# Optimization experiments

Hardware: AMD Instinct MI355X
Metric: run time of the kernel (lower is better)

## Reference

```python
import jax, jax.numpy as jnp
import numpy as np

VOCAB, D = 6000, 256  # vocab_size, units
B, L = 64, 2048


def setup_inputs() -> dict:
    key = jax.random.key(0)
    k1, k2, k3, k4, k5 = jax.random.split(key, 5)
    context = jax.random.randint(k1, (B, L), 0, VOCAB)  # 0 = pad/mask id
    emb = jax.random.normal(k2, (VOCAB, D), dtype=jnp.float32) * 0.05
    # Keras LSTM packs gates as [i, f, c, o] along the last axis (4*D)
    W = jax.random.normal(k3, (D, 4 * D), dtype=jnp.float32) * (1.0 / np.sqrt(D))
    U = jax.random.normal(k4, (D, 4 * D), dtype=jnp.float32) * (1.0 / np.sqrt(D))
    b = jnp.concatenate([
        jnp.zeros((D,), jnp.float32),
        jnp.ones((D,), jnp.float32),   # unit_forget_bias=True default in Keras
        jnp.zeros((2 * D,), jnp.float32),
    ])
    return {"context": context, "emb": emb, "W": W, "U": U, "b": b}


def reference(context, emb, W, U, b):
    mask = context != 0                       # (B, L) mask_zero semantics
    x = emb[context]                          # (B, L, D) embedding lookup
    xg = jnp.einsum("bld,dg->blg", x, W) + b  # (B, L, 4D) input-to-gate, precomputed

    h0 = jnp.zeros((context.shape[0], D), xg.dtype)
    c0 = h0

    def step(carry, inp):
        h, c = carry
        xg_t, m = inp                          # (B, 4D), (B,)
        g = xg_t + h @ U                       # (B, 4D)
        i, f, cand, o = jnp.split(g, 4, axis=-1)
        i = jax.nn.sigmoid(i)
        f = jax.nn.sigmoid(f)
        o = jax.nn.sigmoid(o)
        c_new = f * c + i * jnp.tanh(cand)
        h_new = o * jnp.tanh(c_new)
        m = m[:, None]
        # Keras masking: masked steps carry previous state/output forward
        h = jnp.where(m, h_new, h)
        c = jnp.where(m, c_new, c)
        return (h, c), h

    xs = (jnp.swapaxes(xg, 0, 1), jnp.swapaxes(mask, 0, 1))  # time-major for scan
    (_, _), hs = jax.lax.scan(step, (h0, c0), xs)
    return jnp.swapaxes(hs, 0, 1)             # (B, L, D)
```

## Files before the change

### kernel.cpp

```cpp
#include <hip/hip_runtime.h>
#include <hip/hip_bf16.h>


#define B_     64
#define L_     2048
#define D_     256
#define G4_    1024
#define VOCAB_ 6000

typedef short    s16x8 __attribute__((ext_vector_type(8)));
typedef float    f32x4 __attribute__((ext_vector_type(4)));
typedef unsigned u32x2 __attribute__((ext_vector_type(2)));
typedef unsigned u32x4 __attribute__((ext_vector_type(4)));

#define OFF_EMBB   0u
#define OFF_WT     3072000u
#define OFF_UF     3596288u
#define OFF_HTAG   4120576u
#define OFF_DONE   4251648u
#define OFF_XG     4251712u
#define WS_NEED    272687168u

#define ULDS_OFF   0
#define SG_OFF     65536
#define HL_OFF     82432
#define ROLE_OFF   90624
#define SMEM_TOTAL 90752

__global__ void prep_kernel(const float* __restrict__ emb,
                            const float* __restrict__ W,
                            const float* __restrict__ U,
                            __hip_bfloat16* __restrict__ embb,
                            __hip_bfloat16* __restrict__ Wt,
                            __hip_bfloat16* __restrict__ Ufrag) {
  const int stride = gridDim.x * blockDim.x;
  const int i0 = blockIdx.x * blockDim.x + threadIdx.x;
  for (int i = i0; i < VOCAB_ * D_; i += stride)
    embb[i] = __float2bfloat16(emb[i]);
  for (int i = i0; i < D_ * G4_; i += stride) {
    int k = i >> 10;
    int n = i & (G4_ - 1);
    Wt[n * D_ + k] = __float2bfloat16(W[i]);
  }
  for (int i = i0; i < 262144; i += stride) {
    int j  = i & 7;
    int l  = (i >> 3) & 63;
    int fr = i >> 9;
    int nt = fr & 1;
    int kk = (fr >> 1) & 7;
    int w  = (fr >> 4) & 7;
    int qq = fr >> 7;
    int n = (w >> 1) * 256 + qq * 64 + (w & 1) * 32 + nt * 16 + (l & 15);
    int k = kk * 32 + (l >> 4) * 8 + j;
    Ufrag[i] = __float2bfloat16(U[k * G4_ + n]);
  }
}

__global__ void mask_kernel(const int* __restrict__ ctx,
                            unsigned char* __restrict__ m8) {
  const int stride = gridDim.x * blockDim.x;
  for (int i = blockIdx.x * blockDim.x + threadIdx.x; i < B_ * L_; i += stride) {
    int b = i & 63, t = i >> 6;
    m8[t * 64 + b] = (ctx[b * L_ + t] != 0) ? 1 : 0;
  }
}

__device__ inline unsigned pk2(float a, float b) {
  return (unsigned)__bfloat16_as_ushort(__float2bfloat16(a)) |
         ((unsigned)__bfloat16_as_ushort(__float2bfloat16(b)) << 16);
}
__device__ inline float bl(unsigned u) {
  union { unsigned u; float f; } c; c.u = u << 16; return c.f;
}
__device__ inline float bh(unsigned u) {
  union { unsigned u; float f; } c; c.u = u & 0xffff0000u; return c.f;
}
__device__ inline float fsigmoid(float x) { return 1.f / (1.f + __expf(-x)); }
__device__ inline float ftanh(float x)    { return 1.f - 2.f / (__expf(2.f * x) + 1.f); }

__global__ __launch_bounds__(256, 2)
void xg_kernel(const int* __restrict__ ctx,
               const __hip_bfloat16* __restrict__ embb,
               const __hip_bfloat16* __restrict__ Wt,
               unsigned* __restrict__ xgw) {
  const int bid = blockIdx.x;
  const int Q   = bid & 3;
  const int g   = (bid >> 2) & 3;
  const int tc  = bid >> 4;
  const int tid = threadIdx.x;
  const int wv  = tid >> 6;
  const int l   = tid & 63;
  const int l15 = l & 15, lhi = l >> 4;
  const int row0 = g * 16;

  s16x8 bfr[8][4];
#pragma unroll
  for (int nt = 0; nt < 4; ++nt) {
    const int n = Q * 256 + wv * 64 + nt * 16 + l15;
    const __hip_bfloat16* wp = Wt + n * D_ + lhi * 8;
#pragma unroll
    for (int kk = 0; kk < 8; ++kk)
      bfr[kk][nt] = *(const s16x8*)(wp + kk * 32);
  }

  for (int tt = 0; tt < 64; ++tt) {
    const int t = tc * 64 + tt;
    const int tok = ctx[(row0 + l15) * L_ + t];
    const __hip_bfloat16* xp = embb + tok * D_ + lhi * 8;
    s16x8 af[8];
#pragma unroll
    for (int kk = 0; kk < 8; ++kk)
      af[kk] = *(const s16x8*)(xp + kk * 32);

    f32x4 acc[4];
#pragma unroll
    for (int nt = 0; nt < 4; ++nt) acc[nt] = (f32x4){0.f, 0.f, 0.f, 0.f};
#pragma unroll
    for (int kk = 0; kk < 8; ++kk)
#pragma unroll
      for (int nt = 0; nt < 4; ++nt)
        acc[nt] = __builtin_amdgcn_mfma_f32_16x16x32_bf16(af[kk], bfr[kk][nt], acc[nt], 0, 0, 0);

#pragma unroll
    for (int nt = 0; nt < 4; ++nt)
#pragma unroll
      for (int r = 0; r < 4; ++r) {
        float nb = __shfl_xor(acc[nt][r], 1);
        if (!(l15 & 1)) {
          unsigned v = pk2(acc[nt][r], nb);
          int em = lhi * 4 + r;
          int p  = nt * 8 + (l15 >> 1);
          size_t idx = ((((size_t)(t * 4 + g) * 4 + wv) * 16 + em) * 32 + p) * 4 + Q;
          xgw[idx] = v;
        }
      }
  }
}

__global__ __launch_bounds__(512, 1)
void scan_kernel(const float* __restrict__ bias,
                 const __hip_bfloat16* __restrict__ Ufrag,
                 const unsigned* __restrict__ xgw,
                 const unsigned char* __restrict__ mask8,
                 unsigned* __restrict__ donef,
                 char* __restrict__ htag,
                 float* __restrict__ out) {
  extern __shared__ __align__(16) char smem[];
  const int bid = blockIdx.x;
  const int tid = threadIdx.x;

  if (bid >= 16) {
    volatile int* hd = (volatile int*)(smem + ROLE_OFF);
    if (tid == 0) *hd = 0;
    __syncthreads();
    float v0 = (float)(tid + 1), v1 = v0 * 1.1f, v2 = v0 * 1.2f, v3 = v0 * 1.3f;
    for (int it = 0; it < (1 << 15); ++it) {
#pragma unroll
      for (int kk = 0; kk < 128; ++kk) {
        v0 = __builtin_fmaf(v0, 1.0000001f, 1.0e-7f);
        v1 = __builtin_fmaf(v1, 1.0000001f, 1.0e-7f);
        v2 = __builtin_fmaf(v2, 1.0000001f, 1.0e-7f);
        v3 = __builtin_fmaf(v3, 1.0000001f, 1.0e-7f);
      }
      if (tid == 0 && (it & 3) == 0) {
        u32x4 fa, fb, fc, fd;
        asm volatile(
            "global_load_dwordx4 %0, %4, off sc0 sc1\n\t"
            "global_load_dwordx4 %1, %4, off offset:16 sc0 sc1\n\t"
            "global_load_dwordx4 %2, %4, off offset:32 sc0 sc1\n\t"
            "global_load_dwordx4 %3, %4, off offset:48 sc0 sc1\n\t"
            "s_waitcnt vmcnt(0)"
            : "=&v"(fa), "=&v"(fb), "=&v"(fc), "=&v"(fd)
            : "v"(donef) : "memory");
        unsigned mn = fa.x;
        mn = fa.y < mn ? fa.y : mn; mn = fa.z < mn ? fa.z : mn; mn = fa.w < mn ? fa.w : mn;
        mn = fb.x < mn ? fb.x : mn; mn = fb.y < mn ? fb.y : mn;
        mn = fb.z < mn ? fb.z : mn; mn = fb.w < mn ? fb.w : mn;
        mn = fc.x < mn ? fc.x : mn; mn = fc.y < mn ? fc.y : mn;
        mn = fc.z < mn ? fc.z : mn; mn = fc.w < mn ? fc.w : mn;
        mn = fd.x < mn ? fd.x : mn; mn = fd.y < mn ? fd.y : mn;
        mn = fd.z < mn ? fd.z : mn; mn = fd.w < mn ? fd.w : mn;
        if (mn != 0u) *hd = 1;
      }
      if (*hd) break;
    }
    asm volatile("" :: "v"(v0), "v"(v1), "v"(v2), "v"(v3));
    return;
  }

  const int g = bid >> 2;
  const int q = bid & 3;
  const int row0 = g * 16;

  const int w   = tid >> 6;
  const int l   = tid & 63;
  const int l15 = l & 15, lhi = l >> 4;
  const int Q   = w >> 1, sgs = w & 1;
  const int em  = tid >> 5;
  const int e5  = tid & 31;

  s16x8* ulds = (s16x8*)(smem + ULDS_OFF);
  float* sg   = (float*)(smem + SG_OFF);
  char*  hl   = smem + HL_OFF;

  const s16x8* ufb = (const s16x8*)Ufrag + (size_t)((q * 8 + w) * 16) * 64;
  s16x8 ur[8];
#pragma unroll
  for (int jf = 0; jf < 8; ++jf)
    ur[jf] = ufb[jf * 64 + l];
#pragma unroll
  for (int jf = 0; jf < 8; ++jf)
    ulds[(w * 8 + jf) * 64 + l] = ufb[(8 + jf) * 64 + l];

  float bq[4][2];
#pragma unroll
  for (int Qq = 0; Qq < 4; ++Qq) {
    bq[Qq][0] = bias[Qq * 256 + q * 64 + 2 * e5];
    bq[Qq][1] = bias[Qq * 256 + q * 64 + 2 * e5 + 1];
  }

  float cc[2] = {0.f, 0.f}, hh[2] = {0.f, 0.f};
  __syncthreads();

  const int prow = w * 2 + (l >> 5);
  const int pswz = (prow & 7) << 4;

  for (int t = 0; t < L_; ++t) {
    const u32x4 xq = *(const u32x4*)(xgw +
        (((((size_t)t * 4 + g) * 4 + q) * 16 + em) * 32 + e5) * 4);
    const unsigned char mk = mask8[t * 64 + row0 + em];

    {
      const char* hp = htag + ((t + 1) & 1) * 65536 + (row0 + prow) * 1024 + (l & 31) * 32;
      const unsigned want = (unsigned)t;
      u32x4 qa, qb;
      int spins = 0;
      while (true) {
        asm volatile("global_load_dwordx4 %0, %2, off sc0 sc1\n\t"
                     "global_load_dwordx4 %1, %2, off offset:16 sc0 sc1\n\t"
                     "s_waitcnt vmcnt(0)"
                     : "=&v"(qa), "=&v"(qb) : "v"(hp) : "memory");
        unsigned mn = qa.y < qa.w ? qa.y : qa.w;
        mn = qb.y < mn ? qb.y : mn;
        mn = qb.w < mn ? qb.w : mn;
        if (__all((int)(mn >= want))) break;
        if (++spins > 16384) break;
      }
      union { unsigned u[4]; s16x8 v; } hcv;
      hcv.u[0] = qa.x; hcv.u[1] = qa.z; hcv.u[2] = qb.x; hcv.u[3] = qb.z;
      *(s16x8*)(hl + prow * 512 + (((l & 31) * 16) ^ pswz)) = hcv.v;
    }
    asm volatile("s_waitcnt lgkmcnt(0)" ::: "memory");
    __builtin_amdgcn_s_barrier();

    f32x4 acc0 = {0.f, 0.f, 0.f, 0.f}, acc1 = {0.f, 0.f, 0.f, 0.f};
    s16x8 hf[8];
#pragma unroll
    for (int kk = 0; kk < 8; ++kk)
      hf[kk] = *(const s16x8*)(hl + l15 * 512 + ((kk * 64 + lhi * 16) ^ ((l15 & 7) << 4)));
#pragma unroll
    for (int kk = 0; kk < 4; ++kk) {
      acc0 = __builtin_amdgcn_mfma_f32_16x16x32_bf16(hf[kk], ur[kk * 2 + 0], acc0, 0, 0, 0);
      acc1 = __builtin_amdgcn_mfma_f32_16x16x32_bf16(hf[kk], ur[kk * 2 + 1], acc1, 0, 0, 0);
    }
#pragma unroll
    for (int kk = 4; kk < 8; ++kk) {
      s16x8 u0 = ulds[(w * 8 + (kk - 4) * 2 + 0) * 64 + l];
      s16x8 u1 = ulds[(w * 8 + (kk - 4) * 2 + 1) * 64 + l];
      acc0 = __builtin_amdgcn_mfma_f32_16x16x32_bf16(hf[kk], u0, acc0, 0, 0, 0);
      acc1 = __builtin_amdgcn_mfma_f32_16x16x32_bf16(hf[kk], u1, acc1, 0, 0, 0);
    }

#pragma unroll
    for (int r = 0; r < 4; ++r) {
      sg[(Q * 16 + lhi * 4 + r) * 66 + sgs * 32 + l15]      = acc0[r];
      sg[(Q * 16 + lhi * 4 + r) * 66 + sgs * 32 + 16 + l15] = acc1[r];
    }
    asm volatile("s_waitcnt lgkmcnt(0)" ::: "memory");
    __builtin_amdgcn_s_barrier();

    {
      float gv[4][2];
#pragma unroll
      for (int Qq = 0; Qq < 4; ++Qq) {
        gv[Qq][0] = sg[(Qq * 16 + em) * 66 + 2 * e5];
        gv[Qq][1] = sg[(Qq * 16 + em) * 66 + 2 * e5 + 1];
      }
      const bool upd = (mk != 0);
      unsigned short hsv[2];
#pragma unroll
      for (int b = 0; b < 2; ++b) {
        float xi = b ? bh(xq.x) : bl(xq.x);
        float xf = b ? bh(xq.y) : bl(xq.y);
        float xc = b ? bh(xq.z) : bl(xq.z);
        float xo = b ? bh(xq.w) : bl(xq.w);
        float gi = gv[0][b] + xi + bq[0][b];
        float gf = gv[1][b] + xf + bq[1][b];
        float gc = gv[2][b] + xc + bq[2][b];
        float go = gv[3][b] + xo + bq[3][b];
        float i_ = fsigmoid(gi), f_ = fsigmoid(gf), o_ = fsigmoid(go);
        float cn = f_ * cc[b] + i_ * ftanh(gc);
        float hn = o_ * ftanh(cn);
        cc[b] = upd ? cn : cc[b];
        hh[b] = upd ? hn : hh[b];
        hsv[b] = __bfloat16_as_ushort(__float2bfloat16(hh[b]));
      }
      u32x2 gr;
      gr.x = (unsigned)hsv[0] | ((unsigned)hsv[1] << 16);
      gr.y = (unsigned)(t + 1);
      char* pw = htag + (t & 1) * 65536 + (row0 + em) * 1024 + (q * 32 + e5) * 8;
      asm volatile("global_store_dwordx2 %0, %1, off sc0 sc1"
                   :: "v"(pw), "v"(gr) : "memory");
      float* op = out + ((size_t)(row0 + em) * L_ + t) * D_ + q * 64 + 2 * e5;
      op[0] = hh[0];
      op[1] = hh[1];
    }
  }

  if (tid == 0) {
    unsigned one = 1u;
    unsigned* df = donef + bid;
    asm volatile("global_store_dword %0, %1, off sc0 sc1"
                 :: "v"(df), "v"(one) : "memory");
  }
}

extern "C" void kernel_launch(void* const* d_in, const int* in_sizes, int n_in,
                              void* d_out, int out_size, void* d_ws, size_t ws_size,
                              hipStream_t stream) {
  const int*   ctx  = (const int*)d_in[0];
  const float* emb  = (const float*)d_in[1];
  const float* W    = (const float*)d_in[2];
  const float* U    = (const float*)d_in[3];
  const float* bias = (const float*)d_in[4];
  float* out = (float*)d_out;

  char* ws = (char*)d_ws;
  __hip_bfloat16* embb = (__hip_bfloat16*)(ws + OFF_EMBB);
  __hip_bfloat16* Wt   = (__hip_bfloat16*)(ws + OFF_WT);
  __hip_bfloat16* Uf   = (__hip_bfloat16*)(ws + OFF_UF);
  char*           htag = ws + OFF_HTAG;
  unsigned*       donef = (unsigned*)(ws + OFF_DONE);
  unsigned*       xgw  = (unsigned*)(ws + OFF_XG);
  unsigned char*  m8   = (unsigned char*)(ws + OFF_WT);

  hipMemsetAsync(htag, 0, 131072, stream);
  hipMemsetAsync(donef, 0, 64, stream);

  hipFuncSetAttribute((const void*)scan_kernel,
                      hipFuncAttributeMaxDynamicSharedMemorySize, SMEM_TOTAL);

  prep_kernel<<<1024, 256, 0, stream>>>(emb, W, U, embb, Wt, Uf);
  xg_kernel<<<512, 256, 0, stream>>>(ctx, embb, Wt, xgw);
  mask_kernel<<<128, 256, 0, stream>>>(ctx, m8);
  scan_kernel<<<256, 512, SMEM_TOTAL, stream>>>(bias, Uf, xgw, m8, donef, htag, out);
}
```

Before: 4.792 ms.

## Permute U columns so each lane owns all four gates, drop LDS gate exchange

Reorders the U fragment layout so each wave's MFMA output tile holds the i/f/c/o gates for the same hidden units, spread across lane halves. The gate exchange then uses register shuffles (xor 8) instead of writing to LDS and taking a second barrier per timestep. The xg precompute layout is changed to match, and h stores and outputs are written per lane, with a shuffle to pair bf16 values. This removes a per-step barrier and LDS round trip from the serial recurrence, at the cost of more shuffles and narrower, scattered output stores.

```diff
diff --git a/kernel.cpp b/kernel.cpp
--- a/kernel.cpp
+++ b/kernel.cpp
@@ -21,11 +21,10 @@
 #define OFF_XG     4251712u
 #define WS_NEED    272687168u
 
-#define ULDS_OFF   0
-#define SG_OFF     65536
-#define HL_OFF     82432
-#define ROLE_OFF   90624
-#define SMEM_TOTAL 90752
+#define SMEM_U     65536
+#define HL_OFF     65536
+#define ROLE_OFF   73728
+#define SMEM_TOTAL 73744
 
 __global__ void prep_kernel(const float* __restrict__ emb,
                             const float* __restrict__ W,
@@ -46,11 +45,11 @@
     int j  = i & 7;
     int l  = (i >> 3) & 63;
     int fr = i >> 9;
-    int nt = fr & 1;
-    int kk = (fr >> 1) & 7;
-    int w  = (fr >> 4) & 7;
+    int kk = fr & 7;
+    int st = (fr >> 3) & 1;
+    int wv = (fr >> 4) & 7;
     int qq = fr >> 7;
-    int n = (w >> 1) * 256 + qq * 64 + (w & 1) * 32 + nt * 16 + (l & 15);
+    int n = (st * 2 + ((l & 15) >> 3)) * 256 + qq * 64 + wv * 8 + ((l & 15) & 7);
     int k = kk * 32 + (l >> 4) * 8 + j;
     Ufrag[i] = __float2bfloat16(U[k * G4_ + n]);
   }
@@ -82,7 +81,7 @@
 void xg_kernel(const int* __restrict__ ctx,
                const __hip_bfloat16* __restrict__ embb,
                const __hip_bfloat16* __restrict__ Wt,
-               unsigned* __restrict__ xgw) {
+               char* __restrict__ xgb) {
   const int bid = blockIdx.x;
   const int Q   = bid & 3;
   const int g   = (bid >> 2) & 3;
@@ -122,25 +121,21 @@
         acc[nt] = __builtin_amdgcn_mfma_f32_16x16x32_bf16(af[kk], bfr[kk][nt], acc[nt], 0, 0, 0);
 
 #pragma unroll
-    for (int nt = 0; nt < 4; ++nt)
-#pragma unroll
-      for (int r = 0; r < 4; ++r) {
-        float nb = __shfl_xor(acc[nt][r], 1);
-        if (!(l15 & 1)) {
-          unsigned v = pk2(acc[nt][r], nb);
-          int em = lhi * 4 + r;
-          int p  = nt * 8 + (l15 >> 1);
-          size_t idx = ((((size_t)(t * 4 + g) * 4 + wv) * 16 + em) * 32 + p) * 4 + Q;
-          xgw[idx] = v;
-        }
-      }
+    for (int nt = 0; nt < 4; ++nt) {
+      const int d = wv * 64 + nt * 16 + l15;
+      u32x2 vv;
+      vv.x = pk2(acc[nt][0], acc[nt][1]);
+      vv.y = pk2(acc[nt][2], acc[nt][3]);
+      char* p = xgb + ((((size_t)(t * 4 + g) * 256 + d) * 4 + Q) * 16 + lhi * 4) * 2;
+      *(u32x2*)p = vv;
+    }
   }
 }
 
 __global__ __launch_bounds__(512, 1)
 void scan_kernel(const float* __restrict__ bias,
                  const __hip_bfloat16* __restrict__ Ufrag,
-                 const unsigned* __restrict__ xgw,
+                 const char* __restrict__ xgb,
                  const unsigned char* __restrict__ mask8,
                  unsigned* __restrict__ donef,
                  char* __restrict__ htag,
@@ -191,44 +186,48 @@
   const int g = bid >> 2;
   const int q = bid & 3;
   const int row0 = g * 16;
-
   const int w   = tid >> 6;
   const int l   = tid & 63;
   const int l15 = l & 15, lhi = l >> 4;
-  const int Q   = w >> 1, sgs = w & 1;
-  const int em  = tid >> 5;
-  const int e5  = tid & 31;
-
-  s16x8* ulds = (s16x8*)(smem + ULDS_OFF);
-  float* sg   = (float*)(smem + SG_OFF);
+  const int dd   = l15 & 7;
+  const int dloc = q * 64 + w * 8 + dd;
+  const bool lo  = (l15 < 8);
+
+  s16x8* ulds = (s16x8*)smem;
   char*  hl   = smem + HL_OFF;
-
-  const s16x8* ufb = (const s16x8*)Ufrag + (size_t)((q * 8 + w) * 16) * 64;
+  const s16x8* uf = (const s16x8*)Ufrag;
+
   s16x8 ur[8];
 #pragma unroll
-  for (int jf = 0; jf < 8; ++jf)
-    ur[jf] = ufb[jf * 64 + l];
-#pragma unroll
-  for (int jf = 0; jf < 8; ++jf)
-    ulds[(w * 8 + jf) * 64 + l] = ufb[(8 + jf) * 64 + l];
-
-  float bq[4][2];
-#pragma unroll
-  for (int Qq = 0; Qq < 4; ++Qq) {
-    bq[Qq][0] = bias[Qq * 256 + q * 64 + 2 * e5];
-    bq[Qq][1] = bias[Qq * 256 + q * 64 + 2 * e5 + 1];
-  }
-
-  float cc[2] = {0.f, 0.f}, hh[2] = {0.f, 0.f};
+  for (int kk = 0; kk < 4; ++kk)
+#pragma unroll
+    for (int st = 0; st < 2; ++st)
+      ur[kk * 2 + st] = uf[((((q * 8 + w) * 2 + st) * 8) + kk) * 64 + l];
+#pragma unroll
+  for (int m = 0; m < 8; ++m) {
+    const int st = m & 1, kk = 4 + (m >> 1);
+    ulds[(w * 8 + m) * 64 + l] = uf[((((q * 8 + w) * 2 + st) * 8) + kk) * 64 + l];
+  }
+
+  float bQ[4];
+#pragma unroll
+  for (int Qq = 0; Qq < 4; ++Qq) bQ[Qq] = bias[Qq * 256 + dloc];
+
+  float cst[2] = {0.f, 0.f};
+  float hst[2] = {0.f, 0.f};
+
   __syncthreads();
 
   const int prow = w * 2 + (l >> 5);
   const int pswz = (prow & 7) << 4;
 
   for (int t = 0; t < L_; ++t) {
-    const u32x4 xq = *(const u32x4*)(xgw +
-        (((((size_t)t * 4 + g) * 4 + q) * 16 + em) * 32 + e5) * 4);
-    const unsigned char mk = mask8[t * 64 + row0 + em];
+    const char* xb = xgb + (((size_t)(t * 4 + g) * 256 + dloc) * 64 + lhi * 4) * 2;
+    u32x2 xv0 = *(const u32x2*)(xb);
+    u32x2 xv1 = *(const u32x2*)(xb + 32);
+    u32x2 xv2 = *(const u32x2*)(xb + 64);
+    u32x2 xv3 = *(const u32x2*)(xb + 96);
+    const unsigned mu = *(const unsigned*)(mask8 + t * 64 + row0 + lhi * 4);
 
     {
       const char* hp = htag + ((t + 1) & 1) * 65536 + (row0 + prow) * 1024 + (l & 31) * 32;
@@ -253,67 +252,66 @@
     asm volatile("s_waitcnt lgkmcnt(0)" ::: "memory");
     __builtin_amdgcn_s_barrier();
 
-    f32x4 acc0 = {0.f, 0.f, 0.f, 0.f}, acc1 = {0.f, 0.f, 0.f, 0.f};
+    f32x4 a0 = {0.f, 0.f, 0.f, 0.f}, a1 = {0.f, 0.f, 0.f, 0.f};
     s16x8 hf[8];
 #pragma unroll
     for (int kk = 0; kk < 8; ++kk)
       hf[kk] = *(const s16x8*)(hl + l15 * 512 + ((kk * 64 + lhi * 16) ^ ((l15 & 7) << 4)));
 #pragma unroll
     for (int kk = 0; kk < 4; ++kk) {
-      acc0 = __builtin_amdgcn_mfma_f32_16x16x32_bf16(hf[kk], ur[kk * 2 + 0], acc0, 0, 0, 0);
-      acc1 = __builtin_amdgcn_mfma_f32_16x16x32_bf16(hf[kk], ur[kk * 2 + 1], acc1, 0, 0, 0);
+      a0 = __builtin_amdgcn_mfma_f32_16x16x32_bf16(hf[kk], ur[kk * 2 + 0], a0, 0, 0, 0);
+      a1 = __builtin_amdgcn_mfma_f32_16x16x32_bf16(hf[kk], ur[kk * 2 + 1], a1, 0, 0, 0);
     }
 #pragma unroll
     for (int kk = 4; kk < 8; ++kk) {
       s16x8 u0 = ulds[(w * 8 + (kk - 4) * 2 + 0) * 64 + l];
       s16x8 u1 = ulds[(w * 8 + (kk - 4) * 2 + 1) * 64 + l];
-      acc0 = __builtin_amdgcn_mfma_f32_16x16x32_bf16(hf[kk], u0, acc0, 0, 0, 0);
-      acc1 = __builtin_amdgcn_mfma_f32_16x16x32_bf16(hf[kk], u1, acc1, 0, 0, 0);
-    }
-
-#pragma unroll
-    for (int r = 0; r < 4; ++r) {
-      sg[(Q * 16 + lhi * 4 + r) * 66 + sgs * 32 + l15]      = acc0[r];
-      sg[(Q * 16 + lhi * 4 + r) * 66 + sgs * 32 + 16 + l15] = acc1[r];
-    }
-    asm volatile("s_waitcnt lgkmcnt(0)" ::: "memory");
-    __builtin_amdgcn_s_barrier();
-
-    {
-      float gv[4][2];
-#pragma unroll
-      for (int Qq = 0; Qq < 4; ++Qq) {
-        gv[Qq][0] = sg[(Qq * 16 + em) * 66 + 2 * e5];
-        gv[Qq][1] = sg[(Qq * 16 + em) * 66 + 2 * e5 + 1];
+      a0 = __builtin_amdgcn_mfma_f32_16x16x32_bf16(hf[kk], u0, a0, 0, 0, 0);
+      a1 = __builtin_amdgcn_mfma_f32_16x16x32_bf16(hf[kk], u1, a1, 0, 0, 0);
+    }
+
+#pragma unroll
+    for (int e = 0; e < 2; ++e) {
+      float p0A = __shfl_xor(a0[e], 8);
+      float p0B = __shfl_xor(a0[2 + e], 8);
+      float p1A = __shfl_xor(a1[e], 8);
+      float p1B = __shfl_xor(a1[2 + e], 8);
+      float gi = lo ? a0[e]     : p0B;
+      float gf = lo ? p0A       : a0[2 + e];
+      float gc = lo ? a1[e]     : p1B;
+      float go = lo ? p1A       : a1[2 + e];
+      const int rsel = lo ? e : 2 + e;
+      unsigned w0 = lo ? xv0.x : xv0.y;
+      unsigned w1 = lo ? xv1.x : xv1.y;
+      unsigned w2 = lo ? xv2.x : xv2.y;
+      unsigned w3 = lo ? xv3.x : xv3.y;
+      float xi = e ? bh(w0) : bl(w0);
+      float xf = e ? bh(w1) : bl(w1);
+      float xc = e ? bh(w2) : bl(w2);
+      float xo = e ? bh(w3) : bl(w3);
+      gi += xi + bQ[0];
+      gf += xf + bQ[1];
+      gc += xc + bQ[2];
+      go += xo + bQ[3];
+      float i_ = fsigmoid(gi), f_ = fsigmoid(gf), o_ = fsigmoid(go);
+      float cn = f_ * cst[e] + i_ * ftanh(gc);
+      float hn = o_ * ftanh(cn);
+      const bool upd = ((mu >> (8 * rsel)) & 255u) != 0u;
+      cst[e] = upd ? cn : cst[e];
+      hst[e] = upd ? hn : hst[e];
+
+      float hpair = __shfl_xor(hst[e], 1);
+      const int row = row0 + lhi * 4 + rsel;
+      if (!(dd & 1)) {
+        u32x2 gr;
+        gr.x = pk2(hst[e], hpair);
+        gr.y = (unsigned)(t + 1);
+        char* pw = htag + (t & 1) * 65536 + row * 1024 +
+                   (q * 32 + w * 4 + (dd >> 1)) * 8;
+        asm volatile("global_store_dwordx2 %0, %1, off sc0 sc1"
+                     :: "v"(pw), "v"(gr) : "memory");
       }
-      const bool upd = (mk != 0);
-      unsigned short hsv[2];
-#pragma unroll
-      for (int b = 0; b < 2; ++b) {
-        float xi = b ? bh(xq.x) : bl(xq.x);
-        float xf = b ? bh(xq.y) : bl(xq.y);
-        float xc = b ? bh(xq.z) : bl(xq.z);
-        float xo = b ? bh(xq.w) : bl(xq.w);
-        float gi = gv[0][b] + xi + bq[0][b];
-        float gf = gv[1][b] + xf + bq[1][b];
-        float gc = gv[2][b] + xc + bq[2][b];
-        float go = gv[3][b] + xo + bq[3][b];
-        float i_ = fsigmoid(gi), f_ = fsigmoid(gf), o_ = fsigmoid(go);
-        float cn = f_ * cc[b] + i_ * ftanh(gc);
-        float hn = o_ * ftanh(cn);
-        cc[b] = upd ? cn : cc[b];
-        hh[b] = upd ? hn : hh[b];
-        hsv[b] = __bfloat16_as_ushort(__float2bfloat16(hh[b]));
-      }
-      u32x2 gr;
-      gr.x = (unsigned)hsv[0] | ((unsigned)hsv[1] << 16);
-      gr.y = (unsigned)(t + 1);
-      char* pw = htag + (t & 1) * 65536 + (row0 + em) * 1024 + (q * 32 + e5) * 8;
-      asm volatile("global_store_dwordx2 %0, %1, off sc0 sc1"
-                   :: "v"(pw), "v"(gr) : "memory");
-      float* op = out + ((size_t)(row0 + em) * L_ + t) * D_ + q * 64 + 2 * e5;
-      op[0] = hh[0];
-      op[1] = hh[1];
+      out[((size_t)row * L_ + t) * D_ + dloc] = hst[e];
     }
   }
 
@@ -341,7 +339,7 @@
   __hip_bfloat16* Uf   = (__hip_bfloat16*)(ws + OFF_UF);
   char*           htag = ws + OFF_HTAG;
   unsigned*       donef = (unsigned*)(ws + OFF_DONE);
-  unsigned*       xgw  = (unsigned*)(ws + OFF_XG);
+  char*           xgb  = ws + OFF_XG;
   unsigned char*  m8   = (unsigned char*)(ws + OFF_WT);
 
   hipMemsetAsync(htag, 0, 131072, stream);
@@ -351,7 +349,7 @@
                       hipFuncAttributeMaxDynamicSharedMemorySize, SMEM_TOTAL);
 
   prep_kernel<<<1024, 256, 0, stream>>>(emb, W, U, embb, Wt, Uf);
-  xg_kernel<<<512, 256, 0, stream>>>(ctx, embb, Wt, xgw);
+  xg_kernel<<<512, 256, 0, stream>>>(ctx, embb, Wt, xgb);
   mask_kernel<<<128, 256, 0, stream>>>(ctx, m8);
-  scan_kernel<<<256, 512, SMEM_TOTAL, stream>>>(bias, Uf, xgw, m8, donef, htag, out);
-}
+  scan_kernel<<<256, 512, SMEM_TOTAL, stream>>>(bias, Uf, xgb, m8, donef, htag, out);
+}
```

Result: slower. 9.416 ms (+96.5%).

## Interleave two batch groups per block to hide cross-block h exchange latency

Applied to the files above, without the earlier changes.

Each scan block now owns two 16-row batch groups, cutting the compute blocks from 16 to 8, and processes them alternately within each time step. While group A's gates are computed, group B's hidden state from the other blocks is already in flight. The full U slice for the block is held in registers (16 fragments), which removes the per-step LDS reads of U, and the fragment layout in prep changes to match. The cost is twice the serial work per block per step and higher register pressure, in exchange for more latency hiding and fewer blocks taking part in the inter-block sync.

```diff
diff --git a/kernel.cpp b/kernel.cpp
--- a/kernel.cpp
+++ b/kernel.cpp
@@ -21,11 +21,11 @@
 #define OFF_XG     4251712u
 #define WS_NEED    272687168u
 
-#define ULDS_OFF   0
-#define SG_OFF     65536
-#define HL_OFF     82432
-#define ROLE_OFF   90624
-#define SMEM_TOTAL 90752
+#define HLA_OFF    0
+#define HLB_OFF    8192
+#define SG_OFF     16384
+#define ROLE_OFF   33280
+#define SMEM_TOTAL 90112
 
 __global__ void prep_kernel(const float* __restrict__ emb,
                             const float* __restrict__ W,
@@ -46,11 +46,11 @@
     int j  = i & 7;
     int l  = (i >> 3) & 63;
     int fr = i >> 9;
-    int nt = fr & 1;
-    int kk = (fr >> 1) & 7;
+    int kk = fr & 7;
+    int st = (fr >> 3) & 1;
     int w  = (fr >> 4) & 7;
     int qq = fr >> 7;
-    int n = (w >> 1) * 256 + qq * 64 + (w & 1) * 32 + nt * 16 + (l & 15);
+    int n = (w >> 1) * 256 + qq * 64 + (w & 1) * 32 + st * 16 + (l & 15);
     int k = kk * 32 + (l >> 4) * 8 + j;
     Ufrag[i] = __float2bfloat16(U[k * G4_ + n]);
   }
@@ -149,7 +149,7 @@
   const int bid = blockIdx.x;
   const int tid = threadIdx.x;
 
-  if (bid >= 16) {
+  if (bid >= 8) {
     volatile int* hd = (volatile int*)(smem + ROLE_OFF);
     if (tid == 0) *hd = 0;
     __syncthreads();
@@ -163,23 +163,16 @@
         v3 = __builtin_fmaf(v3, 1.0000001f, 1.0e-7f);
       }
       if (tid == 0 && (it & 3) == 0) {
-        u32x4 fa, fb, fc, fd;
+        u32x4 fa, fb;
         asm volatile(
-            "global_load_dwordx4 %0, %4, off sc0 sc1\n\t"
-            "global_load_dwordx4 %1, %4, off offset:16 sc0 sc1\n\t"
-            "global_load_dwordx4 %2, %4, off offset:32 sc0 sc1\n\t"
-            "global_load_dwordx4 %3, %4, off offset:48 sc0 sc1\n\t"
+            "global_load_dwordx4 %0, %2, off sc0 sc1\n\t"
+            "global_load_dwordx4 %1, %2, off offset:16 sc0 sc1\n\t"
             "s_waitcnt vmcnt(0)"
-            : "=&v"(fa), "=&v"(fb), "=&v"(fc), "=&v"(fd)
-            : "v"(donef) : "memory");
+            : "=&v"(fa), "=&v"(fb) : "v"(donef) : "memory");
         unsigned mn = fa.x;
         mn = fa.y < mn ? fa.y : mn; mn = fa.z < mn ? fa.z : mn; mn = fa.w < mn ? fa.w : mn;
         mn = fb.x < mn ? fb.x : mn; mn = fb.y < mn ? fb.y : mn;
         mn = fb.z < mn ? fb.z : mn; mn = fb.w < mn ? fb.w : mn;
-        mn = fc.x < mn ? fc.x : mn; mn = fc.y < mn ? fc.y : mn;
-        mn = fc.z < mn ? fc.z : mn; mn = fc.w < mn ? fc.w : mn;
-        mn = fd.x < mn ? fd.x : mn; mn = fd.y < mn ? fd.y : mn;
-        mn = fd.z < mn ? fd.z : mn; mn = fd.w < mn ? fd.w : mn;
         if (mn != 0u) *hd = 1;
       }
       if (*hd) break;
@@ -188,9 +181,10 @@
     return;
   }
 
-  const int g = bid >> 2;
-  const int q = bid & 3;
-  const int row0 = g * 16;
+  const int q  = bid & 3;
+  const int pr = bid >> 2;
+  const int gA = pr * 2, gB = pr * 2 + 1;
+  const int row0A = gA * 16, row0B = gB * 16;
 
   const int w   = tid >> 6;
   const int l   = tid & 63;
@@ -199,18 +193,17 @@
   const int em  = tid >> 5;
   const int e5  = tid & 31;
 
-  s16x8* ulds = (s16x8*)(smem + ULDS_OFF);
-  float* sg   = (float*)(smem + SG_OFF);
-  char*  hl   = smem + HL_OFF;
-
-  const s16x8* ufb = (const s16x8*)Ufrag + (size_t)((q * 8 + w) * 16) * 64;
-  s16x8 ur[8];
-#pragma unroll
-  for (int jf = 0; jf < 8; ++jf)
-    ur[jf] = ufb[jf * 64 + l];
-#pragma unroll
-  for (int jf = 0; jf < 8; ++jf)
-    ulds[(w * 8 + jf) * 64 + l] = ufb[(8 + jf) * 64 + l];
+  float* sg  = (float*)(smem + SG_OFF);
+  char*  hlA = smem + HLA_OFF;
+  char*  hlB = smem + HLB_OFF;
+  const s16x8* uf = (const s16x8*)Ufrag;
+
+  s16x8 ur[16];
+#pragma unroll
+  for (int kk = 0; kk < 8; ++kk)
+#pragma unroll
+    for (int st = 0; st < 2; ++st)
+      ur[kk * 2 + st] = uf[((((q * 8 + w) * 2 + st) * 8) + kk) * 64 + l];
 
   float bq[4][2];
 #pragma unroll
@@ -219,62 +212,76 @@
     bq[Qq][1] = bias[Qq * 256 + q * 64 + 2 * e5 + 1];
   }
 
-  float cc[2] = {0.f, 0.f}, hh[2] = {0.f, 0.f};
-  __syncthreads();
+  float cA[2] = {0.f, 0.f}, hA[2] = {0.f, 0.f};
+  float cB[2] = {0.f, 0.f}, hB[2] = {0.f, 0.f};
 
   const int prow = w * 2 + (l >> 5);
   const int pswz = (prow & 7) << 4;
+  const int swzf = (l15 & 7) << 4;
 
   for (int t = 0; t < L_; ++t) {
-    const u32x4 xq = *(const u32x4*)(xgw +
-        (((((size_t)t * 4 + g) * 4 + q) * 16 + em) * 32 + e5) * 4);
-    const unsigned char mk = mask8[t * 64 + row0 + em];
-
-    {
-      const char* hp = htag + ((t + 1) & 1) * 65536 + (row0 + prow) * 1024 + (l & 31) * 32;
-      const unsigned want = (unsigned)t;
-      u32x4 qa, qb;
-      int spins = 0;
-      while (true) {
-        asm volatile("global_load_dwordx4 %0, %2, off sc0 sc1\n\t"
-                     "global_load_dwordx4 %1, %2, off offset:16 sc0 sc1\n\t"
-                     "s_waitcnt vmcnt(0)"
-                     : "=&v"(qa), "=&v"(qb) : "v"(hp) : "memory");
-        unsigned mn = qa.y < qa.w ? qa.y : qa.w;
-        mn = qb.y < mn ? qb.y : mn;
-        mn = qb.w < mn ? qb.w : mn;
-        if (__all((int)(mn >= want))) break;
-        if (++spins > 16384) break;
+    const unsigned want = (unsigned)t;
+    const int par = (t + 1) & 1;
+
+    const char* hpA = htag + par * 65536 + (row0A + prow) * 1024 + (l & 31) * 32;
+    const char* hpB = htag + par * 65536 + (row0B + prow) * 1024 + (l & 31) * 32;
+    u32x4 pa0, pa1, pb0, pb1;
+    asm volatile("global_load_dwordx4 %0, %2, off sc0 sc1\n\t"
+                 "global_load_dwordx4 %1, %2, off offset:16 sc0 sc1"
+                 : "=&v"(pa0), "=&v"(pa1) : "v"(hpA) : "memory");
+    asm volatile("global_load_dwordx4 %0, %2, off sc0 sc1\n\t"
+                 "global_load_dwordx4 %1, %2, off offset:16 sc0 sc1"
+                 : "=&v"(pb0), "=&v"(pb1) : "v"(hpB) : "memory");
+
+    const u32x4 xqA = *(const u32x4*)(xgw +
+        (((((size_t)t * 4 + gA) * 4 + q) * 16 + em) * 32 + e5) * 4);
+    const u32x4 xqB = *(const u32x4*)(xgw +
+        (((((size_t)t * 4 + gB) * 4 + q) * 16 + em) * 32 + e5) * 4);
+    const unsigned char mkA = mask8[t * 64 + row0A + em];
+    const unsigned char mkB = mask8[t * 64 + row0B + em];
+
+    asm volatile("s_waitcnt vmcnt(0)" ::: "memory");
+    {
+      unsigned mn = pa0.y < pa0.w ? pa0.y : pa0.w;
+      mn = pa1.y < mn ? pa1.y : mn;
+      mn = pa1.w < mn ? pa1.w : mn;
+      if (!__all((int)(mn >= want))) {
+        int spins = 0;
+        while (true) {
+          asm volatile("global_load_dwordx4 %0, %2, off sc0 sc1\n\t"
+                       "global_load_dwordx4 %1, %2, off offset:16 sc0 sc1\n\t"
+                       "s_waitcnt vmcnt(0)"
+                       : "=&v"(pa0), "=&v"(pa1) : "v"(hpA) : "memory");
+          mn = pa0.y < pa0.w ? pa0.y : pa0.w;
+          mn = pa1.y < mn ? pa1.y : mn;
+          mn = pa1.w < mn ? pa1.w : mn;
+          if (__all((int)(mn >= want))) break;
+          if (++spins > 16384) break;
+        }
       }
       union { unsigned u[4]; s16x8 v; } hcv;
-      hcv.u[0] = qa.x; hcv.u[1] = qa.z; hcv.u[2] = qb.x; hcv.u[3] = qb.z;
-      *(s16x8*)(hl + prow * 512 + (((l & 31) * 16) ^ pswz)) = hcv.v;
+      hcv.u[0] = pa0.x; hcv.u[1] = pa0.z; hcv.u[2] = pa1.x; hcv.u[3] = pa1.z;
+      *(s16x8*)(hlA + prow * 512 + (((l & 31) * 16) ^ pswz)) = hcv.v;
     }
     asm volatile("s_waitcnt lgkmcnt(0)" ::: "memory");
     __builtin_amdgcn_s_barrier();
 
-    f32x4 acc0 = {0.f, 0.f, 0.f, 0.f}, acc1 = {0.f, 0.f, 0.f, 0.f};
-    s16x8 hf[8];
-#pragma unroll
-    for (int kk = 0; kk < 8; ++kk)
-      hf[kk] = *(const s16x8*)(hl + l15 * 512 + ((kk * 64 + lhi * 16) ^ ((l15 & 7) << 4)));
-#pragma unroll
-    for (int kk = 0; kk < 4; ++kk) {
-      acc0 = __builtin_amdgcn_mfma_f32_16x16x32_bf16(hf[kk], ur[kk * 2 + 0], acc0, 0, 0, 0);
-      acc1 = __builtin_amdgcn_mfma_f32_16x16x32_bf16(hf[kk], ur[kk * 2 + 1], acc1, 0, 0, 0);
-    }
-#pragma unroll
-    for (int kk = 4; kk < 8; ++kk) {
-      s16x8 u0 = ulds[(w * 8 + (kk - 4) * 2 + 0) * 64 + l];
-      s16x8 u1 = ulds[(w * 8 + (kk - 4) * 2 + 1) * 64 + l];
-      acc0 = __builtin_amdgcn_mfma_f32_16x16x32_bf16(hf[kk], u0, acc0, 0, 0, 0);
-      acc1 = __builtin_amdgcn_mfma_f32_16x16x32_bf16(hf[kk], u1, acc1, 0, 0, 0);
-    }
-
-#pragma unroll
-    for (int r = 0; r < 4; ++r) {
-      sg[(Q * 16 + lhi * 4 + r) * 66 + sgs * 32 + l15]      = acc0[r];
-      sg[(Q * 16 + lhi * 4 + r) * 66 + sgs * 32 + 16 + l15] = acc1[r];
+    {
+      f32x4 ac0 = {0.f, 0.f, 0.f, 0.f}, ac1 = {0.f, 0.f, 0.f, 0.f};
+      s16x8 hf[8];
+#pragma unroll
+      for (int kk = 0; kk < 8; ++kk)
+        hf[kk] = *(const s16x8*)(hlA + l15 * 512 + ((kk * 64 + lhi * 16) ^ swzf));
+#pragma unroll
+      for (int kk = 0; kk < 8; ++kk) {
+        ac0 = __builtin_amdgcn_mfma_f32_16x16x32_bf16(hf[kk], ur[kk * 2 + 0], ac0, 0, 0, 0);
+        ac1 = __builtin_amdgcn_mfma_f32_16x16x32_bf16(hf[kk], ur[kk * 2 + 1], ac1, 0, 0, 0);
+      }
+#pragma unroll
+      for (int r = 0; r < 4; ++r) {
+        sg[(Q * 16 + lhi * 4 + r) * 66 + sgs * 32 + l15]      = ac0[r];
+        sg[(Q * 16 + lhi * 4 + r) * 66 + sgs * 32 + 16 + l15] = ac1[r];
+      }
     }
     asm volatile("s_waitcnt lgkmcnt(0)" ::: "memory");
     __builtin_amdgcn_s_barrier();
@@ -286,34 +293,117 @@
         gv[Qq][0] = sg[(Qq * 16 + em) * 66 + 2 * e5];
         gv[Qq][1] = sg[(Qq * 16 + em) * 66 + 2 * e5 + 1];
       }
-      const bool upd = (mk != 0);
+      const bool upd = (mkA != 0);
       unsigned short hsv[2];
 #pragma unroll
       for (int b = 0; b < 2; ++b) {
-        float xi = b ? bh(xq.x) : bl(xq.x);
-        float xf = b ? bh(xq.y) : bl(xq.y);
-        float xc = b ? bh(xq.z) : bl(xq.z);
-        float xo = b ? bh(xq.w) : bl(xq.w);
+        float xi = b ? bh(xqA.x) : bl(xqA.x);
+        float xf = b ? bh(xqA.y) : bl(xqA.y);
+        float xc = b ? bh(xqA.z) : bl(xqA.z);
+        float xo = b ? bh(xqA.w) : bl(xqA.w);
         float gi = gv[0][b] + xi + bq[0][b];
         float gf = gv[1][b] + xf + bq[1][b];
         float gc = gv[2][b] + xc + bq[2][b];
         float go = gv[3][b] + xo + bq[3][b];
         float i_ = fsigmoid(gi), f_ = fsigmoid(gf), o_ = fsigmoid(go);
-        float cn = f_ * cc[b] + i_ * ftanh(gc);
+        float cn = f_ * cA[b] + i_ * ftanh(gc);
         float hn = o_ * ftanh(cn);
-        cc[b] = upd ? cn : cc[b];
-        hh[b] = upd ? hn : hh[b];
-        hsv[b] = __bfloat16_as_ushort(__float2bfloat16(hh[b]));
+        cA[b] = upd ? cn : cA[b];
+        hA[b] = upd ? hn : hA[b];
+        hsv[b] = __bfloat16_as_ushort(__float2bfloat16(hA[b]));
       }
       u32x2 gr;
       gr.x = (unsigned)hsv[0] | ((unsigned)hsv[1] << 16);
       gr.y = (unsigned)(t + 1);
-      char* pw = htag + (t & 1) * 65536 + (row0 + em) * 1024 + (q * 32 + e5) * 8;
+      char* pw = htag + (t & 1) * 65536 + (row0A + em) * 1024 + (q * 32 + e5) * 8;
       asm volatile("global_store_dwordx2 %0, %1, off sc0 sc1"
                    :: "v"(pw), "v"(gr) : "memory");
-      float* op = out + ((size_t)(row0 + em) * L_ + t) * D_ + q * 64 + 2 * e5;
-      op[0] = hh[0];
-      op[1] = hh[1];
+      float* op = out + ((size_t)(row0A + em) * L_ + t) * D_ + q * 64 + 2 * e5;
+      op[0] = hA[0];
+      op[1] = hA[1];
+    }
+
+    asm volatile("s_waitcnt vmcnt(0)" ::: "memory");
+    {
+      unsigned mn = pb0.y < pb0.w ? pb0.y : pb0.w;
+      mn = pb1.y < mn ? pb1.y : mn;
+      mn = pb1.w < mn ? pb1.w : mn;
+      if (!__all((int)(mn >= want))) {
+        int spins = 0;
+        while (true) {
+          asm volatile("global_load_dwordx4 %0, %2, off sc0 sc1\n\t"
+                       "global_load_dwordx4 %1, %2, off offset:16 sc0 sc1\n\t"
+                       "s_waitcnt vmcnt(0)"
+                       : "=&v"(pb0), "=&v"(pb1) : "v"(hpB) : "memory");
+          mn = pb0.y < pb0.w ? pb0.y : pb0.w;
+          mn = pb1.y < mn ? pb1.y : mn;
+          mn = pb1.w < mn ? pb1.w : mn;
+          if (__all((int)(mn >= want))) break;
+          if (++spins > 16384) break;
+        }
+      }
+      union { unsigned u[4]; s16x8 v; } hcv;
+      hcv.u[0] = pb0.x; hcv.u[1] = pb0.z; hcv.u[2] = pb1.x; hcv.u[3] = pb1.z;
+      *(s16x8*)(hlB + prow * 512 + (((l & 31) * 16) ^ pswz)) = hcv.v;
+    }
+    asm volatile("s_waitcnt lgkmcnt(0)" ::: "memory");
+    __builtin_amdgcn_s_barrier();
+
+    {
+      f32x4 ac0 = {0.f, 0.f, 0.f, 0.f}, ac1 = {0.f, 0.f, 0.f, 0.f};
+      s16x8 hf[8];
+#pragma unroll
+      for (int kk = 0; kk < 8; ++kk)
+        hf[kk] = *(const s16x8*)(hlB + l15 * 512 + ((kk * 64 + lhi * 16) ^ swzf));
+#pragma unroll
+      for (int kk = 0; kk < 8; ++kk) {
+        ac0 = __builtin_amdgcn_mfma_f32_16x16x32_bf16(hf[kk], ur[kk * 2 + 0], ac0, 0, 0, 0);
+        ac1 = __builtin_amdgcn_mfma_f32_16x16x32_bf16(hf[kk], ur[kk * 2 + 1], ac1, 0, 0, 0);
+      }
+#pragma unroll
+      for (int r = 0; r < 4; ++r) {
+        sg[(Q * 16 + lhi * 4 + r) * 66 + sgs * 32 + l15]      = ac0[r];
+        sg[(Q * 16 + lhi * 4 + r) * 66 + sgs * 32 + 16 + l15] = ac1[r];
+      }
+    }
+    asm volatile("s_waitcnt lgkmcnt(0)" ::: "memory");
+    __builtin_amdgcn_s_barrier();
+
+    {
+      float gv[4][2];
+#pragma unroll
+      for (int Qq = 0; Qq < 4; ++Qq) {
+        gv[Qq][0] = sg[(Qq * 16 + em) * 66 + 2 * e5];
+        gv[Qq][1] = sg[(Qq * 16 + em) * 66 + 2 * e5 + 1];
+      }
+      const bool upd = (mkB != 0);
+      unsigned short hsv[2];
+#pragma unroll
+      for (int b = 0; b < 2; ++b) {
+        float xi = b ? bh(xqB.x) : bl(xqB.x);
+        float xf = b ? bh(xqB.y) : bl(xqB.y);
+        float xc = b ? bh(xqB.z) : bl(xqB.z);
+        float xo = b ? bh(xqB.w) : bl(xqB.w);
+        float gi = gv[0][b] + xi + bq[0][b];
+        float gf = gv[1][b] + xf + bq[1][b];
+        float gc = gv[2][b] + xc + bq[2][b];
+        float go = gv[3][b] + xo + bq[3][b];
+        float i_ = fsigmoid(gi), f_ = fsigmoid(gf), o_ = fsigmoid(go);
+        float cn = f_ * cB[b] + i_ * ftanh(gc);
+        float hn = o_ * ftanh(cn);
+        cB[b] = upd ? cn : cB[b];
+        hB[b] = upd ? hn : hB[b];
+        hsv[b] = __bfloat16_as_ushort(__float2bfloat16(hB[b]));
+      }
+      u32x2 gr;
+      gr.x = (unsigned)hsv[0] | ((unsigned)hsv[1] << 16);
+      gr.y = (unsigned)(t + 1);
+      char* pw = htag + (t & 1) * 65536 + (row0B + em) * 1024 + (q * 32 + e5) * 8;
+      asm volatile("global_store_dwordx2 %0, %1, off sc0 sc1"
+                   :: "v"(pw), "v"(gr) : "memory");
+      float* op = out + ((size_t)(row0B + em) * L_ + t) * D_ + q * 64 + 2 * e5;
+      op[0] = hB[0];
+      op[1] = hB[1];
     }
   }
 
```

Result: slower. 8.716 ms (+81.9%).
